# Kernel tuning notes

Hardware: AMD Instinct MI355X
Metric: run time of the kernel (lower is better)

The kernel has to match this reference:

```python
import jax, jax.numpy as jnp
import numpy as np

N_NODES = 100000
N_EDGES = 3200000
N_GRAPHS = 512
DIM = 64
NF = 4
BN_EPS = 1e-5

_PARAM_SHAPES = [
    ("c1_w1", (DIM, NF), "randn"), ("c1_b1", (DIM,), "randn"),
    ("c1_g1", (DIM,), "ones"), ("c1_be1", (DIM,), "zeros"),
    ("c1_w2", (DIM, DIM), "randn"), ("c1_b2", (DIM,), "randn"),
    ("bn1_g", (DIM,), "ones"), ("bn1_b", (DIM,), "zeros"),
    ("c2_w1", (DIM, DIM), "randn"), ("c2_b1", (DIM,), "randn"),
    ("c2_g1", (DIM,), "ones"), ("c2_be1", (DIM,), "zeros"),
    ("c2_w2", (DIM, DIM), "randn"), ("c2_b2", (DIM,), "randn"),
    ("bn2_g", (DIM,), "ones"), ("bn2_b", (DIM,), "zeros"),
    ("fc0_w", (DIM, NF), "randn"), ("fc0_b", (DIM,), "randn"),
    ("fc1_w", (DIM, DIM), "randn"), ("fc1_b", (DIM,), "randn"),
    ("fc2_w", (DIM, DIM), "randn"), ("fc2_b", (DIM,), "randn"),
    ("pi_w", (DIM, DIM), "randn"), ("pi_b", (DIM,), "randn"),
    ("vf_w", (DIM, DIM), "randn"), ("vf_b", (DIM,), "randn"),
]


def setup_inputs() -> dict:
    key = jax.random.key(0)
    ks = jax.random.split(key, 3 + len(_PARAM_SHAPES))
    inp = {
        "x": jax.random.normal(ks[0], (N_NODES, NF), jnp.float32),
        "edge_index": jax.random.randint(ks[1], (2, N_EDGES), 0, N_NODES, dtype=jnp.int64)
        if jax.config.jax_enable_x64 else jax.random.randint(ks[1], (2, N_EDGES), 0, N_NODES).astype(jnp.int32),
        "batch": jnp.sort(jax.random.randint(ks[2], (N_NODES,), 0, N_GRAPHS)).astype(jnp.int32),
    }
    for i, (name, shape, fill) in enumerate(_PARAM_SHAPES):
        k = ks[3 + i]
        if fill == "randn":
            inp[name] = jax.random.normal(k, shape, jnp.float32) * 0.1
        elif fill == "ones":
            inp[name] = jnp.ones(shape, jnp.float32)
        else:
            inp[name] = jnp.zeros(shape, jnp.float32)
    return inp


def _lin(x, w, b):
    return x @ w.T + b


def _bn(x, g, b):  # training-mode batch statistics over node axis
    m = x.mean(axis=0)
    v = x.var(axis=0)
    return (x - m) * jax.lax.rsqrt(v + BN_EPS) * g + b


def _gin_conv(x, src, dst, w1, b1, g1, be1, w2, b2):
    # sum-aggregate neighbor messages (GINConv, eps=0): h = MLP(x + sum_{j in N(i)} x_j)
    agg = jax.ops.segment_sum(x[src], dst, num_segments=x.shape[0])
    h = x + agg
    h = jax.nn.relu(_bn(_lin(h, w1, b1), g1, be1))
    return _lin(h, w2, b2)


def reference(x, edge_index, batch,
              c1_w1, c1_b1, c1_g1, c1_be1, c1_w2, c1_b2, bn1_g, bn1_b,
              c2_w1, c2_b1, c2_g1, c2_be1, c2_w2, c2_b2, bn2_g, bn2_b,
              fc0_w, fc0_b, fc1_w, fc1_b, fc2_w, fc2_b,
              pi_w, pi_b, vf_w, vf_b):
    src, dst = edge_index[0], edge_index[1]
    h1 = jax.nn.relu(_bn(_gin_conv(x, src, dst, c1_w1, c1_b1, c1_g1, c1_be1, c1_w2, c1_b2), bn1_g, bn1_b))
    h2 = jax.nn.relu(_bn(_gin_conv(h1, src, dst, c2_w1, c2_b1, c2_g1, c2_be1, c2_w2, c2_b2), bn2_g, bn2_b))
    pool = lambda h: jax.ops.segment_sum(h, batch, num_segments=N_GRAPHS)  # global_add_pool
    # dropout is eval-mode identity
    out = _lin(pool(x), fc0_w, fc0_b) + _lin(pool(h1), fc1_w, fc1_b) + _lin(pool(h2), fc2_w, fc2_b)
    pi = jax.nn.relu(_lin(out, pi_w, pi_b))
    vf = jax.nn.relu(_lin(out, vf_w, vf_b))
    return (pi, vf)
```

## Files before the change

### kernel.cpp

```cpp
#include <hip/hip_runtime.h>

#define N_NODES 100000
#define N_EDGES 3200000
#define N_GRAPHS 512
#define NBKT 782
#define NBLK 256
#define EPB 12500
#define NSCAN 200192
#define NB_SCAN 782
#define SCAP 6000
#define NCOPY 64
#define STREG (NCOPY * 128)

__device__ __forceinline__ uint32_t f2bf(float f) {
  uint32_t u = __float_as_uint(f);
  return (u + 0x7fffu + ((u >> 16) & 1u)) >> 16;
}
__device__ __forceinline__ float bflo(uint32_t u) { return __uint_as_float(u << 16); }
__device__ __forceinline__ float bfhi(uint32_t u) { return __uint_as_float(u & 0xffff0000u); }
__device__ __forceinline__ float rdlane(float v, int lane) {
  return __uint_as_float(__builtin_amdgcn_readlane(__float_as_uint(v), lane));
}

__global__ __launch_bounds__(256) void k_cnt(const int* __restrict__ dst,
                                             int* __restrict__ cnt)
{
  __shared__ int h[NBKT];
  int t = threadIdx.x, blk = blockIdx.x;
  for (int i = t; i < NBKT; i += 256) h[i] = 0;
  __syncthreads();
  int e0 = blk * EPB;
  for (int i = t; i < EPB; i += 256) atomicAdd(&h[dst[e0 + i] >> 7], 1);
  __syncthreads();
  for (int i = t; i < NBKT; i += 256) cnt[i * NBLK + blk] = h[i];
}

__global__ __launch_bounds__(256) void k_scan1(const int* __restrict__ v,
                                               int* __restrict__ bsum, int n)
{
  __shared__ int s[256];
  int i = blockIdx.x * 256 + threadIdx.x;
  s[threadIdx.x] = i < n ? v[i] : 0;
  __syncthreads();
  for (int off = 128; off > 0; off >>= 1) {
    if (threadIdx.x < off) s[threadIdx.x] += s[threadIdx.x + off];
    __syncthreads();
  }
  if (threadIdx.x == 0) bsum[blockIdx.x] = s[0];
}

__global__ void k_scan2(int* __restrict__ bsum, int nb)
{
  __shared__ int s[1024];
  int t = threadIdx.x;
  int v = t < nb ? bsum[t] : 0;
  s[t] = v;
  __syncthreads();
  for (int off = 1; off < 1024; off <<= 1) {
    int nv = t >= off ? s[t - off] : 0;
    __syncthreads();
    s[t] += nv;
    __syncthreads();
  }
  if (t < nb) bsum[t] = s[t] - v;
}

__global__ __launch_bounds__(256) void k_scanout(const int* __restrict__ v,
    const int* __restrict__ boff, int* __restrict__ out, int n)
{
  __shared__ int s[256];
  int t = threadIdx.x, i = blockIdx.x * 256 + t;
  int x = i < n ? v[i] : 0;
  s[t] = x;
  __syncthreads();
  for (int off = 1; off < 256; off <<= 1) {
    int nv = t >= off ? s[t - off] : 0;
    __syncthreads();
    s[t] += nv;
    __syncthreads();
  }
  if (i < n) out[i] = boff[blockIdx.x] + s[t] - x;
}

__global__ __launch_bounds__(256) void k_bin(const int* __restrict__ src,
    const int* __restrict__ dst, const int* __restrict__ off,
    int2* __restrict__ eb)
{
  __shared__ int base[NBKT];
  __shared__ int cur[NBKT];
  int t = threadIdx.x, blk = blockIdx.x;
  for (int i = t; i < NBKT; i += 256) { base[i] = off[i * NBLK + blk]; cur[i] = 0; }
  __syncthreads();
  int e0 = blk * EPB;
  for (int i = t; i < EPB; i += 256) {
    int e = e0 + i;
    int s = src[e], d = dst[e], b = d >> 7;
    int p = atomicAdd(&cur[b], 1);
    eb[base[b] + p] = make_int2(s, d);
  }
}

__global__ __launch_bounds__(256) void k_sortb(const int2* __restrict__ eb,
    const int* __restrict__ off, int* __restrict__ rowstart,
    int* __restrict__ csr)
{
  int b = blockIdx.x, t = threadIdx.x;
  int start = off[b * NBLK];
  int end = (b == NBKT - 1) ? N_EDGES : off[(b + 1) * NBLK];
  int cnt = end - start;
  __shared__ int2 ebs[SCAP];
  __shared__ int h[128], cur[128];
  bool staged = cnt <= SCAP;
  if (staged) for (int i = t; i < cnt; i += 256) ebs[i] = eb[start + i];
  if (t < 128) h[t] = 0;
  __syncthreads();
  if (staged) {
    for (int i = t; i < cnt; i += 256) atomicAdd(&h[ebs[i].y & 127], 1);
  } else {
    for (int i = t; i < cnt; i += 256) atomicAdd(&h[eb[start + i].y & 127], 1);
  }
  __syncthreads();
  int v = t < 128 ? h[t] : 0;
  for (int o = 1; o < 128; o <<= 1) {
    int nv = (t < 128 && t >= o) ? h[t - o] : 0;
    __syncthreads();
    if (t < 128) h[t] += nv;
    __syncthreads();
  }
  if (t < 128) {
    int ex = h[t] - v;
    int node = b * 128 + t;
    if (node < N_NODES) rowstart[node] = start + ex;
    cur[t] = ex;
  }
  if (b == NBKT - 1 && t == 0) rowstart[N_NODES] = N_EDGES;
  __syncthreads();
  if (staged) {
    for (int i = t; i < cnt; i += 256) {
      int2 e = ebs[i];
      int p = atomicAdd(&cur[e.y & 127], 1);
      csr[start + p] = e.x;
    }
  } else {
    for (int i = t; i < cnt; i += 256) {
      int2 e = eb[start + i];
      int p = atomicAdd(&cur[e.y & 127], 1);
      csr[start + p] = e.x;
    }
  }
}

__global__ __launch_bounds__(256) void k_gstart(const int* __restrict__ batch,
                                                int* __restrict__ gstart, int n)
{
  int i = blockIdx.x * 256 + threadIdx.x;
  if (i >= n) return;
  int b = batch[i];
  if (i == 0) {
    for (int g = 0; g <= b; ++g) gstart[g] = 0;
  } else {
    int p = batch[i - 1];
    for (int g = p + 1; g <= b; ++g) gstart[g] = i;
  }
  if (i == n - 1) {
    for (int g = b + 1; g <= N_GRAPHS; ++g) gstart[g] = n;
  }
}

__global__ __launch_bounds__(256) void k_agglin1(const int* __restrict__ csr,
    const int* __restrict__ rowstart, const float* __restrict__ x,
    const float* __restrict__ w1, const float* __restrict__ b1,
    float* __restrict__ OUT, float* __restrict__ st, int n)
{
  __shared__ float sAgg[8][4];
  __shared__ float rs[4][64], rq[4][64];
  int t = threadIdx.x;
  int hw = t >> 5, lane = t & 31;
  int nd = blockIdx.x * 8 + hw;
  const float4* x4 = reinterpret_cast<const float4*>(x);
  float4 a = make_float4(0.f, 0.f, 0.f, 0.f);
  if (nd < n) {
    int e0 = rowstart[nd], e1 = rowstart[nd + 1];
    for (int e = e0 + lane; e < e1; e += 32) {
      float4 v = x4[csr[e]];
      a.x += v.x; a.y += v.y; a.z += v.z; a.w += v.w;
    }
    if (lane == 0) {
      float4 v = x4[nd];
      a.x += v.x; a.y += v.y; a.z += v.z; a.w += v.w;
    }
  }
  for (int off = 1; off < 32; off <<= 1) {
    a.x += __shfl_xor(a.x, off);
    a.y += __shfl_xor(a.y, off);
    a.z += __shfl_xor(a.z, off);
    a.w += __shfl_xor(a.w, off);
  }
  if (lane == 0) *reinterpret_cast<float4*>(&sAgg[hw][0]) = a;
  __syncthreads();
  int d = t & 63, slot = t >> 6;
  float4 wr = reinterpret_cast<const float4*>(w1)[d];
  float bv = b1[d];
  float lsum = 0.f, lsq = 0.f;
  int base = blockIdx.x * 8;
#pragma unroll
  for (int li = slot; li < 8; li += 4) {
    int nn = base + li;
    if (nn < n) {
      float v = bv + sAgg[li][0] * wr.x + sAgg[li][1] * wr.y
                   + sAgg[li][2] * wr.z + sAgg[li][3] * wr.w;
      OUT[nn * 64 + d] = v;
      lsum += v; lsq += v * v;
    }
  }
  rs[slot][d] = lsum; rq[slot][d] = lsq;
  __syncthreads();
  if (t < 64) {
    int cp = (blockIdx.x & (NCOPY - 1)) * 128;
    atomicAdd(&st[cp + d],      rs[0][d] + rs[1][d] + rs[2][d] + rs[3][d]);
    atomicAdd(&st[cp + 64 + d], rq[0][d] + rq[1][d] + rq[2][d] + rq[3][d]);
  }
}

template <bool WRITE_HB>
__global__ __launch_bounds__(256) void k_hpool(const float* __restrict__ T,
    const float* __restrict__ st, const float* __restrict__ gam,
    const float* __restrict__ bet, float invN, const int* __restrict__ batch,
    uint2* __restrict__ Hb, float* __restrict__ pool)
{
  __shared__ float sm[16][64];
  __shared__ int sb[16];
  __shared__ float s_ss[128];
  int t = threadIdx.x;
  int r = t >> 4, c4 = t & 15;
  int row0 = blockIdx.x * 16;
  if (t < 64) {
    float s = 0.f, q = 0.f;
#pragma unroll 8
    for (int c = 0; c < NCOPY; ++c) {
      s += st[c * 128 + t];
      q += st[c * 128 + 64 + t];
    }
    float mean = s * invN;
    float var  = q * invN - mean * mean;
    float sc   = gam[t] * rsqrtf(var + 1e-5f);
    s_ss[t] = sc;
    s_ss[64 + t] = bet[t] - mean * sc;
  }
  if (t >= 64 && t < 80) sb[t - 64] = batch[row0 + t - 64];
  __syncthreads();
  float4 v = reinterpret_cast<const float4*>(T)[(row0 + r) * 16 + c4];
  int c = c4 * 4;
  v.x = fmaxf(v.x * s_ss[c + 0] + s_ss[64 + c + 0], 0.f);
  v.y = fmaxf(v.y * s_ss[c + 1] + s_ss[64 + c + 1], 0.f);
  v.z = fmaxf(v.z * s_ss[c + 2] + s_ss[64 + c + 2], 0.f);
  v.w = fmaxf(v.w * s_ss[c + 3] + s_ss[64 + c + 3], 0.f);
  if (WRITE_HB) {
    uint2 p;
    p.x = f2bf(v.x) | (f2bf(v.y) << 16);
    p.y = f2bf(v.z) | (f2bf(v.w) << 16);
    Hb[(row0 + r) * 16 + c4] = p;
  }
  *reinterpret_cast<float4*>(&sm[r][c]) = v;
  __syncthreads();
  if (t < 64) {
    int gmin = sb[0], gmax = sb[15];
    for (int g = gmin; g <= gmax; ++g) {
      float s = 0.f;
#pragma unroll
      for (int rr = 0; rr < 16; ++rr) if (sb[rr] == g) s += sm[rr][t];
      atomicAdd(&pool[g * 64 + t], s);
    }
  }
}

__global__ __launch_bounds__(256) void k_agg64b(const int* __restrict__ csr,
    const int* __restrict__ rowstart, const uint32_t* __restrict__ Hb,
    float2* __restrict__ AGG, int n)
{
  int hw = threadIdx.x >> 5, lane = threadIdx.x & 31;
  int nd = blockIdx.x * 8 + hw;
  if (nd >= n) return;
  int e = rowstart[nd], e1 = rowstart[nd + 1];
  float a0 = 0.f, a1 = 0.f;
  for (; e + 4 <= e1; e += 4) {
    int s0 = csr[e], s1 = csr[e + 1], s2 = csr[e + 2], s3 = csr[e + 3];
    uint32_t u0 = Hb[s0 * 32 + lane];
    uint32_t u1 = Hb[s1 * 32 + lane];
    uint32_t u2 = Hb[s2 * 32 + lane];
    uint32_t u3 = Hb[s3 * 32 + lane];
    a0 += bflo(u0) + bflo(u1) + bflo(u2) + bflo(u3);
    a1 += bfhi(u0) + bfhi(u1) + bfhi(u2) + bfhi(u3);
  }
  for (; e < e1; ++e) {
    uint32_t u = Hb[csr[e] * 32 + lane];
    a0 += bflo(u); a1 += bfhi(u);
  }
  AGG[nd * 32 + lane] = make_float2(a0, a1);
}

__global__ __launch_bounds__(64) void k_pool_x(const float* __restrict__ x,
    const int* __restrict__ gstart, float* __restrict__ px)
{
  int g = blockIdx.x;
  int r0 = gstart[g], r1 = gstart[g + 1];
  int f = threadIdx.x & 3, slot = threadIdx.x >> 2;
  float acc = 0.f;
  for (int r = r0 + slot; r < r1; r += 16) acc += x[r * 4 + f];
  __shared__ float red[16][4];
  red[slot][f] = acc;
  __syncthreads();
  if (threadIdx.x < 4) {
    float s = 0.f;
    for (int k = 0; k < 16; ++k) s += red[k][f];
    px[g * 4 + f] = s;
  }
}

template <int MODE>
__global__ __launch_bounds__(256) void k_gemm64(const void* __restrict__ IN1,
    const float* __restrict__ IN2, const float* __restrict__ stIn,
    const float* __restrict__ gam, const float* __restrict__ bet, float invN,
    const float* __restrict__ W, const float* __restrict__ bias,
    float* __restrict__ OUT, float* __restrict__ st, int n)
{
  __shared__ float s_ss[128];
  __shared__ float rs[4][64], rq[4][64];
  int tid = threadIdx.x;
  int wav = tid >> 6, lane = tid & 63;
  int rsub = lane >> 4;
  int c4 = lane & 15;
  float4 Wreg[16];
#pragma unroll
  for (int k4 = 0; k4 < 16; k4++)
    Wreg[k4] = reinterpret_cast<const float4*>(W)[lane * 16 + k4];
  float bv = bias[lane];
  if (MODE == 0 && tid < 64) {
    float s = 0.f, q = 0.f;
#pragma unroll 8
    for (int c = 0; c < NCOPY; ++c) {
      s += stIn[c * 128 + tid];
      q += stIn[c * 128 + 64 + tid];
    }
    float mean = s * invN;
    float var  = q * invN - mean * mean;
    float sc   = gam[tid] * rsqrtf(var + 1e-5f);
    s_ss[tid] = sc;
    s_ss[64 + tid] = bet[tid] - mean * sc;
  }
  __syncthreads();
  float4 scv, shv;
  if (MODE == 0) {
    scv = *reinterpret_cast<const float4*>(&s_ss[c4 * 4]);
    shv = *reinterpret_cast<const float4*>(&s_ss[64 + c4 * 4]);
  }
  const float4* in2 = reinterpret_cast<const float4*>(IN2);
  const uint2*  in1 = reinterpret_cast<const uint2*>(IN1);
  float lsum = 0.f, lsq = 0.f;
  int ngroups = n >> 4;
  for (int grp = blockIdx.x; grp < ngroups; grp += gridDim.x) {
    int hrow = grp * 16 + wav * 4 + rsub;
    float4 hv;
    if (MODE == 0) {
      float4 t = in2[hrow * 16 + c4];
      hv.x = fmaxf(t.x * scv.x + shv.x, 0.f);
      hv.y = fmaxf(t.y * scv.y + shv.y, 0.f);
      hv.z = fmaxf(t.z * scv.z + shv.z, 0.f);
      hv.w = fmaxf(t.w * scv.w + shv.w, 0.f);
    } else {
      uint2 hb = in1[hrow * 16 + c4];
      float4 b = in2[hrow * 16 + c4];
      hv.x = bflo(hb.x) + b.x;
      hv.y = bfhi(hb.x) + b.y;
      hv.z = bflo(hb.y) + b.z;
      hv.w = bfhi(hb.y) + b.w;
    }
    float acc[4];
#pragma unroll
    for (int i = 0; i < 4; i++) acc[i] = bv;
#pragma unroll
    for (int k4 = 0; k4 < 16; k4++) {
      float4 w = Wreg[k4];
#pragma unroll
      for (int i = 0; i < 4; i++) {
        int sl = i * 16 + k4;
        acc[i] += rdlane(hv.x, sl) * w.x;
        acc[i] += rdlane(hv.y, sl) * w.y;
        acc[i] += rdlane(hv.z, sl) * w.z;
        acc[i] += rdlane(hv.w, sl) * w.w;
      }
    }
    int rbase = grp * 16 + wav * 4;
#pragma unroll
    for (int i = 0; i < 4; i++) {
      OUT[(rbase + i) * 64 + lane] = acc[i];
      lsum += acc[i]; lsq += acc[i] * acc[i];
    }
  }
  __syncthreads();
  rs[wav][lane] = lsum; rq[wav][lane] = lsq;
  __syncthreads();
  if (tid < 64) {
    int cp = (blockIdx.x & (NCOPY - 1)) * 128;
    atomicAdd(&st[cp + tid],      rs[0][tid] + rs[1][tid] + rs[2][tid] + rs[3][tid]);
    atomicAdd(&st[cp + 64 + tid], rq[0][tid] + rq[1][tid] + rq[2][tid] + rq[3][tid]);
  }
}

__global__ __launch_bounds__(64) void k_head(const float* __restrict__ px,
    const float* __restrict__ ph1, const float* __restrict__ ph2,
    const float* __restrict__ fc0w, const float* __restrict__ fc0b,
    const float* __restrict__ fc1w, const float* __restrict__ fc1b,
    const float* __restrict__ fc2w, const float* __restrict__ fc2b,
    const float* __restrict__ piw, const float* __restrict__ pib,
    const float* __restrict__ vfw, const float* __restrict__ vfb,
    float* __restrict__ out)
{
  int g = blockIdx.x, d = threadIdx.x;
  float o = fc0b[d] + fc1b[d] + fc2b[d];
  float4 pxv = reinterpret_cast<const float4*>(px)[g];
  float4 w0 = reinterpret_cast<const float4*>(fc0w)[d];
  o += pxv.x * w0.x + pxv.y * w0.y + pxv.z * w0.z + pxv.w * w0.w;
  const float4* p1 = reinterpret_cast<const float4*>(ph1) + g * 16;
  const float4* w1 = reinterpret_cast<const float4*>(fc1w) + d * 16;
  const float4* p2 = reinterpret_cast<const float4*>(ph2) + g * 16;
  const float4* w2 = reinterpret_cast<const float4*>(fc2w) + d * 16;
#pragma unroll
  for (int k = 0; k < 16; k++) {
    float4 a = p1[k], b = w1[k];
    o += a.x * b.x + a.y * b.y + a.z * b.z + a.w * b.w;
    float4 c = p2[k], e = w2[k];
    o += c.x * e.x + c.y * e.y + c.z * e.z + c.w * e.w;
  }
  __shared__ float so[64];
  so[d] = o;
  __syncthreads();
  float p = pib[d], v = vfb[d];
  const float4* sov = reinterpret_cast<const float4*>(so);
  const float4* wp = reinterpret_cast<const float4*>(piw) + d * 16;
  const float4* wv = reinterpret_cast<const float4*>(vfw) + d * 16;
#pragma unroll
  for (int k = 0; k < 16; k++) {
    float4 a = sov[k], b = wp[k], c = wv[k];
    p += a.x * b.x + a.y * b.y + a.z * b.z + a.w * b.w;
    v += a.x * c.x + a.y * c.y + a.z * c.z + a.w * c.w;
  }
  out[g * 64 + d] = fmaxf(p, 0.f);
  out[N_GRAPHS * 64 + g * 64 + d] = fmaxf(v, 0.f);
}

extern "C" void kernel_launch(void* const* d_in, const int* in_sizes, int n_in,
                              void* d_out, int out_size, void* d_ws, size_t ws_size,
                              hipStream_t stream)
{
  const float* x     = (const float*)d_in[0];
  const int*   ei    = (const int*)d_in[1];
  const int*   batch = (const int*)d_in[2];
  const float* c1_w1 = (const float*)d_in[3];
  const float* c1_b1 = (const float*)d_in[4];
  const float* c1_g1 = (const float*)d_in[5];
  const float* c1_be1= (const float*)d_in[6];
  const float* c1_w2 = (const float*)d_in[7];
  const float* c1_b2 = (const float*)d_in[8];
  const float* bn1_g = (const float*)d_in[9];
  const float* bn1_b = (const float*)d_in[10];
  const float* c2_w1 = (const float*)d_in[11];
  const float* c2_b1 = (const float*)d_in[12];
  const float* c2_g1 = (const float*)d_in[13];
  const float* c2_be1= (const float*)d_in[14];
  const float* c2_w2 = (const float*)d_in[15];
  const float* c2_b2 = (const float*)d_in[16];
  const float* bn2_g = (const float*)d_in[17];
  const float* bn2_b = (const float*)d_in[18];
  const float* fc0_w = (const float*)d_in[19];
  const float* fc0_b = (const float*)d_in[20];
  const float* fc1_w = (const float*)d_in[21];
  const float* fc1_b = (const float*)d_in[22];
  const float* fc2_w = (const float*)d_in[23];
  const float* fc2_b = (const float*)d_in[24];
  const float* pi_w  = (const float*)d_in[25];
  const float* pi_b  = (const float*)d_in[26];
  const float* vf_w  = (const float*)d_in[27];
  const float* vf_b  = (const float*)d_in[28];
  const int* src = ei;
  const int* dst = ei + N_EDGES;

  float* ws = (float*)d_ws;
  float* stats    = ws;
  float* ph1      = ws + 32768;
  float* ph2      = ws + 65536;
  float* px       = ws + 98304;
  int*   gstart   = (int*)(ws + 100352);
  int*   bsum     = (int*)(ws + 100880);
  int*   rowstart = (int*)(ws + 101920);
  float* U        = ws + 201936;
  int*   cnt      = (int*)U;
  int*   off      = (int*)U + 200192;
  uint32_t* Hb    = (uint32_t*)U;
  int*   csr      = (int*)(ws + 3401936);
  float* A        = ws + 6601936;
  int2*  eb       = (int2*)A;

  const float invN = 1.0f / (float)N_NODES;

  hipMemsetAsync(ws, 0, 98304 * sizeof(float), stream);

  k_cnt    <<<NBLK, 256, 0, stream>>>(dst, cnt);
  k_scan1  <<<NB_SCAN, 256, 0, stream>>>(cnt, bsum, NSCAN);
  k_scan2  <<<1, 1024, 0, stream>>>(bsum, NB_SCAN);
  k_scanout<<<NB_SCAN, 256, 0, stream>>>(cnt, bsum, off, NSCAN);
  k_bin    <<<NBLK, 256, 0, stream>>>(src, dst, off, eb);
  k_sortb  <<<NBKT, 256, 0, stream>>>(eb, off, rowstart, csr);
  k_gstart <<<(N_NODES + 255) / 256, 256, 0, stream>>>(batch, gstart, N_NODES);

  k_pool_x<<<N_GRAPHS, 64, 0, stream>>>(x, gstart, px);

  k_agglin1<<<N_NODES / 8, 256, 0, stream>>>(csr, rowstart, x, c1_w1, c1_b1,
                                             A, stats + 0 * STREG, N_NODES);
  k_gemm64<0><<<1024, 256, 0, stream>>>(nullptr, A, stats + 0 * STREG,
      c1_g1, c1_be1, invN, c1_w2, c1_b2, A, stats + 1 * STREG, N_NODES);
  k_hpool<true><<<N_NODES / 16, 256, 0, stream>>>(A, stats + 1 * STREG, bn1_g, bn1_b,
      invN, batch, (uint2*)Hb, ph1);

  k_agg64b<<<(N_NODES + 7) / 8, 256, 0, stream>>>(csr, rowstart, Hb, (float2*)A, N_NODES);
  k_gemm64<2><<<1024, 256, 0, stream>>>(Hb, A, nullptr,
      nullptr, nullptr, 0.f, c2_w1, c2_b1, A, stats + 2 * STREG, N_NODES);
  k_gemm64<0><<<1024, 256, 0, stream>>>(nullptr, A, stats + 2 * STREG,
      c2_g1, c2_be1, invN, c2_w2, c2_b2, A, stats + 3 * STREG, N_NODES);
  k_hpool<false><<<N_NODES / 16, 256, 0, stream>>>(A, stats + 3 * STREG, bn2_g, bn2_b,
      invN, batch, nullptr, ph2);

  k_head<<<N_GRAPHS, 64, 0, stream>>>(px, ph1, ph2, fc0_w, fc0_b, fc1_w, fc1_b,
                                      fc2_w, fc2_b, pi_w, pi_b, vf_w, vf_b, (float*)d_out);
}
```

Measured before the change: 368.6 us.

## Use bf16 MFMA for the 64x64 dense layers instead of readlane FMAs

The per-node 64x64 linear layers stop broadcasting inputs with readlane and doing scalar FMAs. Each wave now computes a 16-row tile with bf16 16x16x32 MFMA instructions, keeping weights in registers as bf16 fragments. The work split becomes one 16-row group per wave rather than per block, the grid is enlarged to cover all groups, and the BN statistics reduction is adapted to the MFMA output layout. Rounding activations and weights to bf16 adds precision loss and risks tolerance issues, and OUT is written in place over A.

After: 335.5 us. 9.0% less time.

```diff
diff --git a/kernel.cpp b/kernel.cpp
--- a/kernel.cpp
+++ b/kernel.cpp
@@ -12,15 +12,15 @@
 #define NCOPY 64
 #define STREG (NCOPY * 128)
 
+typedef short bf16x8 __attribute__((ext_vector_type(8)));
+typedef float f32x4 __attribute__((ext_vector_type(4)));
+
 __device__ __forceinline__ uint32_t f2bf(float f) {
   uint32_t u = __float_as_uint(f);
   return (u + 0x7fffu + ((u >> 16) & 1u)) >> 16;
 }
 __device__ __forceinline__ float bflo(uint32_t u) { return __uint_as_float(u << 16); }
 __device__ __forceinline__ float bfhi(uint32_t u) { return __uint_as_float(u & 0xffff0000u); }
-__device__ __forceinline__ float rdlane(float v, int lane) {
-  return __uint_as_float(__builtin_amdgcn_readlane(__float_as_uint(v), lane));
-}
 
 __global__ __launch_bounds__(256) void k_cnt(const int* __restrict__ dst,
                                              int* __restrict__ cnt)
@@ -328,13 +328,7 @@
   __shared__ float rs[4][64], rq[4][64];
   int tid = threadIdx.x;
   int wav = tid >> 6, lane = tid & 63;
-  int rsub = lane >> 4;
-  int c4 = lane & 15;
-  float4 Wreg[16];
-#pragma unroll
-  for (int k4 = 0; k4 < 16; k4++)
-    Wreg[k4] = reinterpret_cast<const float4*>(W)[lane * 16 + k4];
-  float bv = bias[lane];
+  int m16 = lane & 15, kb = lane >> 4;
   if (MODE == 0 && tid < 64) {
     float s = 0.f, q = 0.f;
 #pragma unroll 8
@@ -349,56 +343,111 @@
     s_ss[64 + tid] = bet[tid] - mean * sc;
   }
   __syncthreads();
-  float4 scv, shv;
+  float sc0[8], sh0[8], sc1[8], sh1[8];
   if (MODE == 0) {
-    scv = *reinterpret_cast<const float4*>(&s_ss[c4 * 4]);
-    shv = *reinterpret_cast<const float4*>(&s_ss[64 + c4 * 4]);
-  }
+#pragma unroll
+    for (int e = 0; e < 8; e++) {
+      sc0[e] = s_ss[kb * 8 + e];       sh0[e] = s_ss[64 + kb * 8 + e];
+      sc1[e] = s_ss[32 + kb * 8 + e];  sh1[e] = s_ss[96 + kb * 8 + e];
+    }
+  }
+  bf16x8 Bf[4][2];
+#pragma unroll
+  for (int tt = 0; tt < 4; tt++)
+#pragma unroll
+    for (int kh = 0; kh < 2; kh++) {
+      const float* wr = W + (tt * 16 + m16) * 64 + kh * 32 + kb * 8;
+      float4 w0 = *reinterpret_cast<const float4*>(wr);
+      float4 w1 = *reinterpret_cast<const float4*>(wr + 4);
+      bf16x8 f;
+      f[0] = (short)f2bf(w0.x); f[1] = (short)f2bf(w0.y);
+      f[2] = (short)f2bf(w0.z); f[3] = (short)f2bf(w0.w);
+      f[4] = (short)f2bf(w1.x); f[5] = (short)f2bf(w1.y);
+      f[6] = (short)f2bf(w1.z); f[7] = (short)f2bf(w1.w);
+      Bf[tt][kh] = f;
+    }
+  float bvt[4];
+#pragma unroll
+  for (int tt = 0; tt < 4; tt++) bvt[tt] = bias[tt * 16 + m16];
   const float4* in2 = reinterpret_cast<const float4*>(IN2);
   const uint2*  in1 = reinterpret_cast<const uint2*>(IN1);
-  float lsum = 0.f, lsq = 0.f;
+  float lsum[4] = {0.f, 0.f, 0.f, 0.f}, lsq[4] = {0.f, 0.f, 0.f, 0.f};
+  int wid = blockIdx.x * 4 + wav, wstride = gridDim.x * 4;
   int ngroups = n >> 4;
-  for (int grp = blockIdx.x; grp < ngroups; grp += gridDim.x) {
-    int hrow = grp * 16 + wav * 4 + rsub;
-    float4 hv;
+  for (int g = wid; g < ngroups; g += wstride) {
+    int rbase = g * 16;
+    int arow = rbase + m16;
+    float av0[8], av1[8];
     if (MODE == 0) {
-      float4 t = in2[hrow * 16 + c4];
-      hv.x = fmaxf(t.x * scv.x + shv.x, 0.f);
-      hv.y = fmaxf(t.y * scv.y + shv.y, 0.f);
-      hv.z = fmaxf(t.z * scv.z + shv.z, 0.f);
-      hv.w = fmaxf(t.w * scv.w + shv.w, 0.f);
+      float4 q0 = in2[arow * 16 + kb * 2];
+      float4 q1 = in2[arow * 16 + kb * 2 + 1];
+      float4 q2 = in2[arow * 16 + 8 + kb * 2];
+      float4 q3 = in2[arow * 16 + 8 + kb * 2 + 1];
+      float r0[8] = {q0.x, q0.y, q0.z, q0.w, q1.x, q1.y, q1.z, q1.w};
+      float r1[8] = {q2.x, q2.y, q2.z, q2.w, q3.x, q3.y, q3.z, q3.w};
+#pragma unroll
+      for (int e = 0; e < 8; e++) {
+        av0[e] = fmaxf(r0[e] * sc0[e] + sh0[e], 0.f);
+        av1[e] = fmaxf(r1[e] * sc1[e] + sh1[e], 0.f);
+      }
     } else {
-      uint2 hb = in1[hrow * 16 + c4];
-      float4 b = in2[hrow * 16 + c4];
-      hv.x = bflo(hb.x) + b.x;
-      hv.y = bfhi(hb.x) + b.y;
-      hv.z = bflo(hb.y) + b.z;
-      hv.w = bfhi(hb.y) + b.w;
-    }
-    float acc[4];
-#pragma unroll
-    for (int i = 0; i < 4; i++) acc[i] = bv;
-#pragma unroll
-    for (int k4 = 0; k4 < 16; k4++) {
-      float4 w = Wreg[k4];
-#pragma unroll
-      for (int i = 0; i < 4; i++) {
-        int sl = i * 16 + k4;
-        acc[i] += rdlane(hv.x, sl) * w.x;
-        acc[i] += rdlane(hv.y, sl) * w.y;
-        acc[i] += rdlane(hv.z, sl) * w.z;
-        acc[i] += rdlane(hv.w, sl) * w.w;
+      uint2 b0 = in1[arow * 16 + kb * 2];
+      uint2 b1 = in1[arow * 16 + kb * 2 + 1];
+      uint2 b2 = in1[arow * 16 + 8 + kb * 2];
+      uint2 b3 = in1[arow * 16 + 8 + kb * 2 + 1];
+      float4 g0 = in2[arow * 16 + kb * 2];
+      float4 g1 = in2[arow * 16 + kb * 2 + 1];
+      float4 g2 = in2[arow * 16 + 8 + kb * 2];
+      float4 g3 = in2[arow * 16 + 8 + kb * 2 + 1];
+      av0[0] = bflo(b0.x) + g0.x; av0[1] = bfhi(b0.x) + g0.y;
+      av0[2] = bflo(b0.y) + g0.z; av0[3] = bfhi(b0.y) + g0.w;
+      av0[4] = bflo(b1.x) + g1.x; av0[5] = bfhi(b1.x) + g1.y;
+      av0[6] = bflo(b1.y) + g1.z; av0[7] = bfhi(b1.y) + g1.w;
+      av1[0] = bflo(b2.x) + g2.x; av1[1] = bfhi(b2.x) + g2.y;
+      av1[2] = bflo(b2.y) + g2.z; av1[3] = bfhi(b2.y) + g2.w;
+      av1[4] = bflo(b3.x) + g3.x; av1[5] = bfhi(b3.x) + g3.y;
+      av1[6] = bflo(b3.y) + g3.z; av1[7] = bfhi(b3.y) + g3.w;
+    }
+    bf16x8 A0, A1;
+#pragma unroll
+    for (int e = 0; e < 8; e++) {
+      A0[e] = (short)f2bf(av0[e]);
+      A1[e] = (short)f2bf(av1[e]);
+    }
+    f32x4 acc[4];
+#pragma unroll
+    for (int tt = 0; tt < 4; tt++) {
+      acc[tt][0] = bvt[tt]; acc[tt][1] = bvt[tt];
+      acc[tt][2] = bvt[tt]; acc[tt][3] = bvt[tt];
+      acc[tt] = __builtin_amdgcn_mfma_f32_16x16x32_bf16(A0, Bf[tt][0], acc[tt], 0, 0, 0);
+      acc[tt] = __builtin_amdgcn_mfma_f32_16x16x32_bf16(A1, Bf[tt][1], acc[tt], 0, 0, 0);
+    }
+#pragma unroll
+    for (int tt = 0; tt < 4; tt++)
+#pragma unroll
+      for (int r = 0; r < 4; r++) {
+        int row = rbase + kb * 4 + r;
+        float v = acc[tt][r];
+        OUT[row * 64 + tt * 16 + m16] = v;
+        lsum[tt] += v; lsq[tt] += v * v;
       }
-    }
-    int rbase = grp * 16 + wav * 4;
-#pragma unroll
-    for (int i = 0; i < 4; i++) {
-      OUT[(rbase + i) * 64 + lane] = acc[i];
-      lsum += acc[i]; lsq += acc[i] * acc[i];
-    }
-  }
-  __syncthreads();
-  rs[wav][lane] = lsum; rq[wav][lane] = lsq;
+  }
+#pragma unroll
+  for (int tt = 0; tt < 4; tt++) {
+    float s = lsum[tt];
+    s += __shfl_xor(s, 16); s += __shfl_xor(s, 32);
+    lsum[tt] = s;
+    float q = lsq[tt];
+    q += __shfl_xor(q, 16); q += __shfl_xor(q, 32);
+    lsq[tt] = q;
+  }
+  if (lane < 16) {
+#pragma unroll
+    for (int tt = 0; tt < 4; tt++) {
+      rs[wav][tt * 16 + lane] = lsum[tt];
+      rq[wav][tt * 16 + lane] = lsq[tt];
+    }
+  }
   __syncthreads();
   if (tid < 64) {
     int cp = (blockIdx.x & (NCOPY - 1)) * 128;
@@ -517,15 +566,15 @@
 
   k_agglin1<<<N_NODES / 8, 256, 0, stream>>>(csr, rowstart, x, c1_w1, c1_b1,
                                              A, stats + 0 * STREG, N_NODES);
-  k_gemm64<0><<<1024, 256, 0, stream>>>(nullptr, A, stats + 0 * STREG,
+  k_gemm64<0><<<1563, 256, 0, stream>>>(nullptr, A, stats + 0 * STREG,
       c1_g1, c1_be1, invN, c1_w2, c1_b2, A, stats + 1 * STREG, N_NODES);
   k_hpool<true><<<N_NODES / 16, 256, 0, stream>>>(A, stats + 1 * STREG, bn1_g, bn1_b,
       invN, batch, (uint2*)Hb, ph1);
 
   k_agg64b<<<(N_NODES + 7) / 8, 256, 0, stream>>>(csr, rowstart, Hb, (float2*)A, N_NODES);
-  k_gemm64<2><<<1024, 256, 0, stream>>>(Hb, A, nullptr,
+  k_gemm64<2><<<1563, 256, 0, stream>>>(Hb, A, nullptr,
       nullptr, nullptr, 0.f, c2_w1, c2_b1, A, stats + 2 * STREG, N_NODES);
-  k_gemm64<0><<<1024, 256, 0, stream>>>(nullptr, A, stats + 2 * STREG,
+  k_gemm64<0><<<1563, 256, 0, stream>>>(nullptr, A, stats + 2 * STREG,
       c2_g1, c2_be1, invN, c2_w2, c2_b2, A, stats + 3 * STREG, N_NODES);
   k_hpool<false><<<N_NODES / 16, 256, 0, stream>>>(A, stats + 3 * STREG, bn2_g, bn2_b,
       invN, batch, nullptr, ph2);
```
